# Kernel optimization log

Measured on AMD Instinct MI355X. Metric: run time of the kernel, lower is better.

The kernel has to match this reference:

```python
import jax, jax.numpy as jnp
import numpy as np

B, N, H = 4, 4096, 64
T1 = 3072  # num_types = [0, 3072, 1024]


def _xavier(key, shape):
    fan_in, fan_out = shape[1], shape[0]
    lim = float(np.sqrt(6.0 / (fan_in + fan_out)))
    return jax.random.uniform(key, shape, jnp.float32, -lim, lim)


def setup_inputs() -> dict:
    key = jax.random.key(0)
    ks = jax.random.split(key, 16)
    adjacency = (jax.random.uniform(ks[0], (N, N)) < 0.05).astype(jnp.float32)
    adjacency = jnp.maximum(adjacency, jnp.eye(N, dtype=jnp.float32))  # avoid all-zero rows
    return {
        "hidden_states": jax.random.normal(ks[1], (B, N, H), jnp.float32),
        "input_states": jax.random.normal(ks[2], (B, 1, 1), jnp.float32),
        "adjacency": adjacency,
        "Wq": _xavier(ks[3], (H, H)),
        "Wk": _xavier(ks[4], (H, H)),
        "Wv": _xavier(ks[5], (H, H)),
        "Wu_inter": _xavier(ks[6], (H, H)),
        "bu_inter": jnp.zeros((H,), jnp.float32),
        "Wt_inter": _xavier(ks[7], (H, H)),
        "bt_inter": jnp.zeros((H,), jnp.float32),
        "Wu_out": _xavier(ks[8], (H, H)),
        "bu_out": jnp.zeros((H,), jnp.float32),
        "Wt_out": _xavier(ks[9], (H, H)),
        "bt_out": jnp.zeros((H,), jnp.float32),
        "step_size": jnp.float32(0.01),
    }


def reference(hidden_states, input_states, adjacency, Wq, Wk, Wv,
              Wu_inter, bu_inter, Wt_inter, bt_inter,
              Wu_out, bu_out, Wt_out, bt_out, step_size):
    # AccumulatorFunction: adjacency-masked QK^T, L2-norm rows (NOT softmax), aggregate V
    mask = adjacency.T  # [N, N]
    q = hidden_states @ Wq.T  # [B, N, H]
    k = hidden_states @ Wk.T
    v = hidden_states @ Wv.T
    rel = jnp.einsum('bnd,bmd->bnm', q, k) * mask  # [B, N, N]
    rel = rel / jnp.linalg.norm(rel, axis=2, keepdims=True)
    acc = jnp.einsum('bnm,bmd->bnd', rel, v)  # [B, N, H]

    # update_hidden_states with num_types = [0, T1, N - T1]
    def branch(h, a, Wu, bu, Wt, bt):
        dt = 2.0 * jax.nn.sigmoid(h @ Wt.T + bt) - 1.0
        return h + step_size * dt * (a @ Wu.T + bu)

    upd_inter = branch(hidden_states[:, :T1], acc[:, :T1],
                       Wu_inter, bu_inter, Wt_inter, bt_inter)
    upd_out = branch(hidden_states[:, T1:], acc[:, T1:],
                     Wu_out, bu_out, Wt_out, bt_out)
    return jnp.concatenate([upd_inter, upd_out], axis=1)  # [B, N, H]
```

## Files before the change

kernel.cpp:

```cpp
#include <hip/hip_runtime.h>
#include <hip/hip_bf16.h>
#include <math.h>

#define Bb 4
#define Nn 4096
#define Hh 64
#define T1c 3072
#define MC 4

typedef unsigned short ushort_t;
typedef __bf16 bf16x4 __attribute__((ext_vector_type(4)));
typedef __bf16 bf16x8 __attribute__((ext_vector_type(8)));
typedef float floatx4 __attribute__((ext_vector_type(4)));
typedef float floatx16 __attribute__((ext_vector_type(16)));

__device__ ushort_t g_qw[(size_t)Bb * Nn * Hh];
__device__ ushort_t g_kw[(size_t)Bb * Nn * Hh];
__device__ ushort_t g_vt[(size_t)Bb * Nn * Hh];
__device__ ushort_t g_dt[(size_t)Bb * Nn * Hh];
__device__ unsigned long long g_bm[(size_t)Nn * (Nn / 64)];
__device__ float    g_pac[(size_t)Bb * 64 * MC * 64 * 64];
__device__ float    g_pss[(size_t)Bb * 64 * MC * 64];

__device__ __forceinline__ float bf2f(unsigned short u) {
    union { unsigned int i; float f; } c;
    c.i = ((unsigned int)u) << 16;
    return c.f;
}
__device__ __forceinline__ unsigned short f2bf(float f) {
    union { float f; unsigned int i; } c;
    c.f = f;
    unsigned int x = c.i;
    unsigned int r = (x + 0x7fffu + ((x >> 16) & 1u)) >> 16;
    return (unsigned short)r;
}

__device__ __forceinline__ bf16x8 ld8(const void* p, size_t eidx, bool f32) {
    if (f32) {
        const float* fp = (const float*)p + eidx;
        float4 x0 = *(const float4*)fp;
        float4 x1 = *(const float4*)(fp + 4);
        bf16x8 r;
        r[0] = (__bf16)x0.x; r[1] = (__bf16)x0.y; r[2] = (__bf16)x0.z; r[3] = (__bf16)x0.w;
        r[4] = (__bf16)x1.x; r[5] = (__bf16)x1.y; r[6] = (__bf16)x1.z; r[7] = (__bf16)x1.w;
        return r;
    }
    return *(const bf16x8*)((const ushort_t*)p + eidx);
}
__device__ __forceinline__ float ldS(const void* p, size_t eidx, bool f32) {
    return f32 ? ((const float*)p)[eidx] : bf2f(((const ushort_t*)p)[eidx]);
}
__device__ __forceinline__ void stOut(void* p, size_t eidx, float v, bool f32) {
    if (f32) ((float*)p)[eidx] = v;
    else ((ushort_t*)p)[eidx] = f2bf(v);
}

__device__ __forceinline__ floatx4 mfma16(bf16x8 a, bf16x8 b, floatx4 c) {
    return __builtin_amdgcn_mfma_f32_16x16x32_bf16(a, b, c, 0, 0, 0);
}
__device__ __forceinline__ floatx16 mfma32(bf16x8 a, bf16x8 b, floatx16 c) {
    return __builtin_amdgcn_mfma_f32_32x32x16_bf16(a, b, c, 0, 0, 0);
}
__device__ __forceinline__ bf16x8 cat44(bf16x4 lo, bf16x4 hi) {
    bf16x8 r;
    r[0] = lo[0]; r[1] = lo[1]; r[2] = lo[2]; r[3] = lo[3];
    r[4] = hi[0]; r[5] = hi[1]; r[6] = hi[2]; r[7] = hi[3];
    return r;
}

__device__ __forceinline__ float fast_tanh(float x) {
    float e = __expf(-2.0f * fabsf(x));
    float t = (1.0f - e) / (1.0f + e);
    return copysignf(t, x);
}

__global__ __launch_bounds__(256) void qkvt_kernel(
    const void* __restrict__ hid, const void* __restrict__ adj,
    const void* __restrict__ Wq, const void* __restrict__ Wk,
    const void* __restrict__ Wv,
    const void* __restrict__ Wti, const void* __restrict__ bti,
    const void* __restrict__ Wto, const void* __restrict__ bto)
{
    const bool F32 = (*(const unsigned*)adj) == 0x3F800000u;

    const int bi = blockIdx.x;
    const int b = bi >> 8;
    const int n16 = (bi & 255) << 4;
    const int t = threadIdx.x;
    const int wv = t >> 6, lane = t & 63, l16 = lane & 15, quad = lane >> 4;
    const bool inter = (n16 < T1c);

    const void* W = (wv == 0) ? Wq : (wv == 1) ? Wk : (wv == 2) ? Wv
                    : (inter ? Wti : Wto);
    const void* bt = inter ? bti : bto;

    const size_t hbase = ((size_t)(b * Nn + n16 + l16)) * Hh + quad * 8;
    bf16x8 a0 = ld8(hid, hbase, F32);
    bf16x8 a1 = ld8(hid, hbase + 32, F32);
    floatx4 z = {0.f, 0.f, 0.f, 0.f};

    floatx4 c[4];
#pragma unroll
    for (int ti = 0; ti < 4; ++ti) {
        const size_t wrow = (size_t)(ti * 16 + l16) * 64 + quad * 8;
        bf16x8 w0 = ld8(W, wrow, F32);
        bf16x8 w1 = ld8(W, wrow + 32, F32);
        c[ti] = mfma16(a1, w1, mfma16(a0, w0, z));
    }

    if (wv == 0 || wv == 1) {
        ushort_t* dst = (wv == 0) ? g_qw : g_kw;
#pragma unroll
        for (int ti = 0; ti < 4; ++ti)
#pragma unroll
            for (int r = 0; r < 4; ++r)
                dst[((size_t)(b * Nn + n16 + quad * 4 + r)) * 64 + ti * 16 + l16] = f2bf(c[ti][r]);
    } else if (wv == 2) {
#pragma unroll
        for (int ti = 0; ti < 4; ++ti) {
            uint2 pk;
            pk.x = (unsigned)f2bf(c[ti][0]) | ((unsigned)f2bf(c[ti][1]) << 16);
            pk.y = (unsigned)f2bf(c[ti][2]) | ((unsigned)f2bf(c[ti][3]) << 16);
            *(uint2*)&g_vt[((size_t)(b * 64 + ti * 16 + l16)) * Nn + n16 + quad * 4] = pk;
        }
    } else {
#pragma unroll
        for (int ti = 0; ti < 4; ++ti) {
            const float btv = ldS(bt, ti * 16 + l16, F32);
#pragma unroll
            for (int r = 0; r < 4; ++r)
                g_dt[((size_t)(b * Nn + n16 + quad * 4 + r)) * 64 + ti * 16 + l16] =
                    f2bf(fast_tanh(0.5f * (c[ti][r] + btv)));
        }
    }
}

__global__ __launch_bounds__(256) void bm_kernel(const void* __restrict__ adj)
{
    const bool F32 = (*(const unsigned*)adj) == 0x3F800000u;
    const int bi = blockIdx.x;
    const int mt = bi & 63;
    const int nc = bi >> 6;
    const int n = nc * 256 + threadIdx.x;
    const int m0 = mt * 64;

    unsigned long long bits = 0ull;
#pragma unroll 8
    for (int j = 0; j < 64; ++j) {
        const float v = ldS(adj, (size_t)(m0 + j) * Nn + n, F32);
        bits |= (unsigned long long)(v != 0.f) << j;
    }
    g_bm[(size_t)n * 64 + mt] = bits;
}

__global__ __launch_bounds__(256, 4) void attn_part_kernel()
{
    __shared__ __align__(16) unsigned char smem[64 * 72 * 2 * 2 + 256];
    ushort_t* kT  = (ushort_t*)smem;
    ushort_t* vTl = kT + 64 * 72;

    const unsigned* bm32 = (const unsigned*)g_bm;

    const int bi = blockIdx.x;
    const int b  = bi >> 8;
    const int mc = bi & 3;
    const int nt = (bi >> 2) & 63;
    const int n0 = nt << 6;
    const int t = threadIdx.x;
    const int wv = t >> 6, lane = t & 63;
    const int l32 = lane & 31, h = lane >> 5;
    const int nh = wv >> 1, mh = wv & 1;

    bf16x8 qf[4];
#pragma unroll
    for (int i = 0; i < 4; ++i)
        qf[i] = *(const bf16x8*)&g_qw[((size_t)(b * Nn + n0 + nh * 32 + l32)) * 64 + h * 8 + 16 * i];

    floatx16 acc[2];
#pragma unroll
    for (int dt = 0; dt < 2; ++dt)
#pragma unroll
        for (int r = 0; r < 16; ++r) acc[dt][r] = 0.f;
    float ssql = 0.f;

    int srow[2], scol[2];
#pragma unroll
    for (int i = 0; i < 2; ++i) { const int cc = t + 256 * i; srow[i] = cc >> 3; scol[i] = (cc & 7) * 8; }

    for (int it = 0; it < 16; ++it) {
        const int m0 = mc * 1024 + it * 64;

#pragma unroll
        for (int i = 0; i < 2; ++i) {
            *(bf16x8*)&kT[srow[i] * 72 + scol[i]] =
                *(const bf16x8*)&g_kw[((size_t)(b * Nn + m0 + srow[i])) * 64 + scol[i]];
            *(bf16x8*)&vTl[srow[i] * 72 + scol[i]] =
                *(const bf16x8*)&g_vt[((size_t)(b * 64 + srow[i])) * Nn + m0 + scol[i]];
        }
        __syncthreads();

        floatx16 s;
#pragma unroll
        for (int r = 0; r < 16; ++r) s[r] = 0.f;
#pragma unroll
        for (int i = 0; i < 4; ++i) {
            bf16x8 kf = *(const bf16x8*)&kT[(mh * 32 + l32) * 72 + h * 8 + 16 * i];
            s = mfma32(kf, qf[i], s);
        }

        const unsigned mw = bm32[(size_t)(n0 + nh * 32 + l32) * 128 + mc * 32 + it * 2 + mh];
        bf16x8 af0, af1;
#pragma unroll
        for (int r = 0; r < 16; ++r) {
            const int rp = (r & 3) + 8 * (r >> 2) + 4 * h;
            const float sm = ((mw >> rp) & 1u) ? s[r] : 0.f;
            ssql += sm * sm;
            if (r < 8) af0[r] = (__bf16)sm; else af1[r - 8] = (__bf16)sm;
        }

#pragma unroll
        for (int dt = 0; dt < 2; ++dt) {
            const int vrow = (dt * 32 + l32) * 72 + mh * 32 + 4 * h;
            bf16x4 lo0 = *(const bf16x4*)&vTl[vrow];
            bf16x4 hi0 = *(const bf16x4*)&vTl[vrow + 8];
            acc[dt] = mfma32(af0, cat44(lo0, hi0), acc[dt]);
            bf16x4 lo1 = *(const bf16x4*)&vTl[vrow + 16];
            bf16x4 hi1 = *(const bf16x4*)&vTl[vrow + 16 + 8];
            acc[dt] = mfma32(af1, cat44(lo1, hi1), acc[dt]);
        }
        __syncthreads();
    }

    ssql += __shfl_xor(ssql, 32, 64);

    float* accbuf = (float*)smem;
    float* ssqbuf = (float*)(smem + 16384);
    if (mh == 1) {
#pragma unroll
        for (int dt = 0; dt < 2; ++dt)
#pragma unroll
            for (int r = 0; r < 16; ++r) {
                const int rp = (r & 3) + 8 * (r >> 2) + 4 * h;
                accbuf[((size_t)nh * 32 + rp) * 64 + dt * 32 + l32] = acc[dt][r];
            }
        if (h == 0) ssqbuf[nh * 32 + l32] = ssql;
    }
    __syncthreads();
    if (mh == 0) {
        const size_t pbase = ((size_t)(b * 64 + nt) * MC + mc);
#pragma unroll
        for (int dt = 0; dt < 2; ++dt)
#pragma unroll
            for (int r = 0; r < 16; ++r) {
                const int rp = (r & 3) + 8 * (r >> 2) + 4 * h;
                const float v = acc[dt][r] + accbuf[((size_t)nh * 32 + rp) * 64 + dt * 32 + l32];
                g_pac[(pbase * 64 + nh * 32 + rp) * 64 + dt * 32 + l32] = v;
            }
        ssql += ssqbuf[nh * 32 + l32];
        if (h == 0) g_pss[pbase * 64 + nh * 32 + l32] = ssql;
    }
}

__global__ __launch_bounds__(256) void finish_kernel(
    const void* __restrict__ hid, const void* __restrict__ adj,
    const void* __restrict__ Wui, const void* __restrict__ bui,
    const void* __restrict__ Wuo, const void* __restrict__ buo,
    const void* __restrict__ stepp, void* __restrict__ outp)
{
    const bool F32 = (*(const unsigned*)adj) == 0x3F800000u;

    const int bi = blockIdx.x;
    const int b = bi >> 8;
    const int r16 = bi & 255;
    const int n16 = r16 << 4;
    const int nt = r16 >> 2;
    const int nloc0 = (r16 & 3) << 4;
    const int t = threadIdx.x;
    const int wv = t >> 6, lane = t & 63, l16 = lane & 15, quad = lane >> 4;

    const size_t sbase = ((size_t)(b * 64 + nt) * MC + quad) * 64 + nloc0 + l16;
    float sv = g_pss[sbase];
    sv += __shfl_xor(sv, 16, 64);
    sv += __shfl_xor(sv, 32, 64);
    const float inv = (sv > 0.f) ? __frsqrt_rn(sv) : 0.f;

    float s0[8], s1[8];
#pragma unroll
    for (int j = 0; j < 8; ++j) { s0[j] = 0.f; s1[j] = 0.f; }
#pragma unroll
    for (int mcq = 0; mcq < MC; ++mcq) {
        const size_t abase =
            (((size_t)(b * 64 + nt) * MC + mcq) * 64 + nloc0 + l16) * 64 + quad * 8;
        float4 x0 = *(const float4*)&g_pac[abase];
        float4 x1 = *(const float4*)&g_pac[abase + 4];
        float4 y0 = *(const float4*)&g_pac[abase + 32];
        float4 y1 = *(const float4*)&g_pac[abase + 36];
        s0[0] += x0.x; s0[1] += x0.y; s0[2] += x0.z; s0[3] += x0.w;
        s0[4] += x1.x; s0[5] += x1.y; s0[6] += x1.z; s0[7] += x1.w;
        s1[0] += y0.x; s1[1] += y0.y; s1[2] += y0.z; s1[3] += y0.w;
        s1[4] += y1.x; s1[5] += y1.y; s1[6] += y1.z; s1[7] += y1.w;
    }
    bf16x8 ua0, ua1;
#pragma unroll
    for (int j = 0; j < 8; ++j) {
        ua0[j] = (__bf16)(s0[j] * inv);
        ua1[j] = (__bf16)(s1[j] * inv);
    }

    const bool inter = (n16 < T1c);
    const void* Wu = inter ? Wui : Wuo;
    const void* bu = inter ? bui : buo;
    const float step = ldS(stepp, 0, F32);

    const int ti = wv;
    floatx4 z = {0.f, 0.f, 0.f, 0.f};
    const size_t wrow = (size_t)(ti * 16 + l16) * 64 + quad * 8;
    bf16x8 w0 = ld8(Wu, wrow, F32);
    bf16x8 w1 = ld8(Wu, wrow + 32, F32);
    floatx4 u = mfma16(ua1, w1, mfma16(ua0, w0, z));
    const float buv = ldS(bu, ti * 16 + l16, F32);
#pragma unroll
    for (int r = 0; r < 4; ++r) {
        const size_t idx = ((size_t)(b * Nn + n16 + quad * 4 + r)) * 64 + ti * 16 + l16;
        const float hv = ldS(hid, idx, F32);
        const float dtv = bf2f(g_dt[idx]);
        stOut(outp, idx, hv + step * dtv * (u[r] + buv), F32);
    }
}

extern "C" void kernel_launch(void* const* d_in, const int* in_sizes, int n_in,
                              void* d_out, int out_size, void* d_ws, size_t ws_size,
                              hipStream_t stream)
{
    const void* hid = d_in[0];
    const void* adj = d_in[2];
    const void* Wq  = d_in[3];
    const void* Wk  = d_in[4];
    const void* Wv  = d_in[5];
    const void* Wui = d_in[6];
    const void* bui = d_in[7];
    const void* Wti = d_in[8];
    const void* bti = d_in[9];
    const void* Wuo = d_in[10];
    const void* buo = d_in[11];
    const void* Wto = d_in[12];
    const void* bto = d_in[13];
    const void* stepp = d_in[14];

    qkvt_kernel<<<dim3(Bb * (Nn / 16)), dim3(256), 0, stream>>>(
        hid, adj, Wq, Wk, Wv, Wti, bti, Wto, bto);
    bm_kernel<<<dim3(1024), dim3(256), 0, stream>>>(adj);
    attn_part_kernel<<<dim3(Bb * 64 * MC), dim3(256), 0, stream>>>();
    finish_kernel<<<dim3(Bb * (Nn / 16)), dim3(256), 0, stream>>>(
        hid, adj, Wui, bui, Wuo, buo, stepp, d_out);
}
```

Before: 182.9 us.

## Pre-pack K and V in MFMA fragment layout and drop LDS staging in attention

The QKV projection now writes K and V into a packed layout that matches the MFMA operand fragments. Each wave in the attention kernel then loads its K/V operands straight from global memory, with no LDS staging, no __syncthreads and no cross-wave reduction through shared memory. Each wave owns its own 32 query rows, and the key range is split into 8 chunks instead of 4 to keep 1024 blocks. This removes barriers and LDS traffic. In exchange, every wave re-reads K/V from global memory or L2, and the finish kernel has twice as many partials to sum.

```diff
diff --git a/kernel.cpp b/kernel.cpp
--- a/kernel.cpp
+++ b/kernel.cpp
@@ -6,17 +6,16 @@
 #define Nn 4096
 #define Hh 64
 #define T1c 3072
-#define MC 4
+#define MC 8
 
 typedef unsigned short ushort_t;
-typedef __bf16 bf16x4 __attribute__((ext_vector_type(4)));
 typedef __bf16 bf16x8 __attribute__((ext_vector_type(8)));
 typedef float floatx4 __attribute__((ext_vector_type(4)));
 typedef float floatx16 __attribute__((ext_vector_type(16)));
 
 __device__ ushort_t g_qw[(size_t)Bb * Nn * Hh];
-__device__ ushort_t g_kw[(size_t)Bb * Nn * Hh];
-__device__ ushort_t g_vt[(size_t)Bb * Nn * Hh];
+__device__ ushort_t g_kp[(size_t)Bb * Nn * Hh];
+__device__ ushort_t g_vp[(size_t)Bb * Nn * Hh];
 __device__ ushort_t g_dt[(size_t)Bb * Nn * Hh];
 __device__ unsigned long long g_bm[(size_t)Nn * (Nn / 64)];
 __device__ float    g_pac[(size_t)Bb * 64 * MC * 64 * 64];
@@ -61,12 +60,6 @@
 __device__ __forceinline__ floatx16 mfma32(bf16x8 a, bf16x8 b, floatx16 c) {
     return __builtin_amdgcn_mfma_f32_32x32x16_bf16(a, b, c, 0, 0, 0);
 }
-__device__ __forceinline__ bf16x8 cat44(bf16x4 lo, bf16x4 hi) {
-    bf16x8 r;
-    r[0] = lo[0]; r[1] = lo[1]; r[2] = lo[2]; r[3] = lo[3];
-    r[4] = hi[0]; r[5] = hi[1]; r[6] = hi[2]; r[7] = hi[3];
-    return r;
-}
 
 __device__ __forceinline__ float fast_tanh(float x) {
     float e = __expf(-2.0f * fabsf(x));
@@ -108,20 +101,37 @@
         c[ti] = mfma16(a1, w1, mfma16(a0, w0, z));
     }
 
-    if (wv == 0 || wv == 1) {
-        ushort_t* dst = (wv == 0) ? g_qw : g_kw;
+    if (wv == 0) {
 #pragma unroll
         for (int ti = 0; ti < 4; ++ti)
 #pragma unroll
             for (int r = 0; r < 4; ++r)
-                dst[((size_t)(b * Nn + n16 + quad * 4 + r)) * 64 + ti * 16 + l16] = f2bf(c[ti][r]);
+                g_qw[((size_t)(b * Nn + n16 + quad * 4 + r)) * 64 + ti * 16 + l16] = f2bf(c[ti][r]);
+    } else if (wv == 1) {
+#pragma unroll
+        for (int ti = 0; ti < 4; ++ti) {
+            const int d = ti * 16 + l16;
+#pragma unroll
+            for (int r = 0; r < 4; ++r) {
+                const int m = n16 + quad * 4 + r;
+                const size_t idx =
+                    ((((size_t)(b * 128 + (m >> 5)) * 4 + (d >> 4)) * 2 + ((d >> 3) & 1)) * 32
+                     + (m & 31)) * 8 + (d & 7);
+                g_kp[idx] = f2bf(c[ti][r]);
+            }
+        }
     } else if (wv == 2) {
 #pragma unroll
         for (int ti = 0; ti < 4; ++ti) {
-            uint2 pk;
-            pk.x = (unsigned)f2bf(c[ti][0]) | ((unsigned)f2bf(c[ti][1]) << 16);
-            pk.y = (unsigned)f2bf(c[ti][2]) | ((unsigned)f2bf(c[ti][3]) << 16);
-            *(uint2*)&g_vt[((size_t)(b * 64 + ti * 16 + l16)) * Nn + n16 + quad * 4] = pk;
+            const int d = ti * 16 + l16;
+#pragma unroll
+            for (int r = 0; r < 4; ++r) {
+                const int m = n16 + quad * 4 + r;
+                const size_t idx =
+                    ((((size_t)(b * 256 + (m >> 4)) * 2 + (d >> 5)) * 2 + ((m >> 2) & 1)) * 32
+                     + (d & 31)) * 8 + ((m & 3) | ((m >> 1) & 4));
+                g_vp[idx] = f2bf(c[ti][r]);
+            }
         }
     } else {
 #pragma unroll
@@ -155,26 +165,21 @@
 
 __global__ __launch_bounds__(256, 4) void attn_part_kernel()
 {
-    __shared__ __align__(16) unsigned char smem[64 * 72 * 2 * 2 + 256];
-    ushort_t* kT  = (ushort_t*)smem;
-    ushort_t* vTl = kT + 64 * 72;
-
     const unsigned* bm32 = (const unsigned*)g_bm;
 
     const int bi = blockIdx.x;
     const int b  = bi >> 8;
-    const int mc = bi & 3;
-    const int nt = (bi >> 2) & 63;
-    const int n0 = nt << 6;
-    const int t = threadIdx.x;
-    const int wv = t >> 6, lane = t & 63;
+    const int mc = (bi >> 5) & 7;
+    const int jq = bi & 31;
+    const int wv = threadIdx.x >> 6, lane = threadIdx.x & 63;
     const int l32 = lane & 31, h = lane >> 5;
-    const int nh = wv >> 1, mh = wv & 1;
+    const int j = jq * 4 + wv;
+    const int n0w = j * 32;
 
     bf16x8 qf[4];
 #pragma unroll
     for (int i = 0; i < 4; ++i)
-        qf[i] = *(const bf16x8*)&g_qw[((size_t)(b * Nn + n0 + nh * 32 + l32)) * 64 + h * 8 + 16 * i];
+        qf[i] = *(const bf16x8*)&g_qw[((size_t)(b * Nn + n0w + l32)) * 64 + h * 8 + 16 * i];
 
     floatx16 acc[2];
 #pragma unroll
@@ -183,32 +188,20 @@
         for (int r = 0; r < 16; ++r) acc[dt][r] = 0.f;
     float ssql = 0.f;
 
-    int srow[2], scol[2];
-#pragma unroll
-    for (int i = 0; i < 2; ++i) { const int cc = t + 256 * i; srow[i] = cc >> 3; scol[i] = (cc & 7) * 8; }
-
     for (int it = 0; it < 16; ++it) {
-        const int m0 = mc * 1024 + it * 64;
-
-#pragma unroll
-        for (int i = 0; i < 2; ++i) {
-            *(bf16x8*)&kT[srow[i] * 72 + scol[i]] =
-                *(const bf16x8*)&g_kw[((size_t)(b * Nn + m0 + srow[i])) * 64 + scol[i]];
-            *(bf16x8*)&vTl[srow[i] * 72 + scol[i]] =
-                *(const bf16x8*)&g_vt[((size_t)(b * 64 + srow[i])) * Nn + m0 + scol[i]];
-        }
-        __syncthreads();
+        const int mb32 = mc * 16 + it;
 
         floatx16 s;
 #pragma unroll
         for (int r = 0; r < 16; ++r) s[r] = 0.f;
 #pragma unroll
         for (int i = 0; i < 4; ++i) {
-            bf16x8 kf = *(const bf16x8*)&kT[(mh * 32 + l32) * 72 + h * 8 + 16 * i];
+            bf16x8 kf = *(const bf16x8*)&g_kp[
+                ((((size_t)(b * 128 + mb32) * 4 + i) * 2 + h) * 32 + l32) * 8];
             s = mfma32(kf, qf[i], s);
         }
 
-        const unsigned mw = bm32[(size_t)(n0 + nh * 32 + l32) * 128 + mc * 32 + it * 2 + mh];
+        const unsigned mw = bm32[(size_t)(n0w + l32) * 128 + mb32];
         bf16x8 af0, af1;
 #pragma unroll
         for (int r = 0; r < 16; ++r) {
@@ -219,46 +212,33 @@
         }
 
 #pragma unroll
-        for (int dt = 0; dt < 2; ++dt) {
-            const int vrow = (dt * 32 + l32) * 72 + mh * 32 + 4 * h;
-            bf16x4 lo0 = *(const bf16x4*)&vTl[vrow];
-            bf16x4 hi0 = *(const bf16x4*)&vTl[vrow + 8];
-            acc[dt] = mfma32(af0, cat44(lo0, hi0), acc[dt]);
-            bf16x4 lo1 = *(const bf16x4*)&vTl[vrow + 16];
-            bf16x4 hi1 = *(const bf16x4*)&vTl[vrow + 16 + 8];
-            acc[dt] = mfma32(af1, cat44(lo1, hi1), acc[dt]);
-        }
-        __syncthreads();
+        for (int mb = 0; mb < 2; ++mb) {
+            const size_t vb = (((size_t)(b * 256 + mb32 * 2 + mb) * 2) * 2 + h) * 32 * 8;
+            bf16x8 vf0 = *(const bf16x8*)&g_vp[vb + (size_t)l32 * 8];
+            bf16x8 vf1 = *(const bf16x8*)&g_vp[vb + (2 * 32 * 8) + (size_t)l32 * 8];
+            if (mb == 0) {
+                acc[0] = mfma32(af0, vf0, acc[0]);
+                acc[1] = mfma32(af0, vf1, acc[1]);
+            } else {
+                acc[0] = mfma32(af1, vf0, acc[0]);
+                acc[1] = mfma32(af1, vf1, acc[1]);
+            }
+        }
     }
 
     ssql += __shfl_xor(ssql, 32, 64);
 
-    float* accbuf = (float*)smem;
-    float* ssqbuf = (float*)(smem + 16384);
-    if (mh == 1) {
-#pragma unroll
-        for (int dt = 0; dt < 2; ++dt)
-#pragma unroll
-            for (int r = 0; r < 16; ++r) {
-                const int rp = (r & 3) + 8 * (r >> 2) + 4 * h;
-                accbuf[((size_t)nh * 32 + rp) * 64 + dt * 32 + l32] = acc[dt][r];
-            }
-        if (h == 0) ssqbuf[nh * 32 + l32] = ssql;
-    }
-    __syncthreads();
-    if (mh == 0) {
-        const size_t pbase = ((size_t)(b * 64 + nt) * MC + mc);
-#pragma unroll
-        for (int dt = 0; dt < 2; ++dt)
-#pragma unroll
-            for (int r = 0; r < 16; ++r) {
-                const int rp = (r & 3) + 8 * (r >> 2) + 4 * h;
-                const float v = acc[dt][r] + accbuf[((size_t)nh * 32 + rp) * 64 + dt * 32 + l32];
-                g_pac[(pbase * 64 + nh * 32 + rp) * 64 + dt * 32 + l32] = v;
-            }
-        ssql += ssqbuf[nh * 32 + l32];
-        if (h == 0) g_pss[pbase * 64 + nh * 32 + l32] = ssql;
-    }
+    const int nt = n0w >> 6;
+    const int nl0 = (j & 1) * 32;
+    const size_t pbase = ((size_t)(b * 64 + nt) * MC + mc);
+#pragma unroll
+    for (int dt = 0; dt < 2; ++dt)
+#pragma unroll
+        for (int r = 0; r < 16; ++r) {
+            const int rp = (r & 3) + 8 * (r >> 2) + 4 * h;
+            g_pac[(pbase * 64 + nl0 + rp) * 64 + dt * 32 + l32] = acc[dt][r];
+        }
+    if (h == 0) g_pss[pbase * 64 + nl0 + l32] = ssql;
 }
 
 __global__ __launch_bounds__(256) void finish_kernel(
@@ -278,15 +258,15 @@
     const int t = threadIdx.x;
     const int wv = t >> 6, lane = t & 63, l16 = lane & 15, quad = lane >> 4;
 
-    const size_t sbase = ((size_t)(b * 64 + nt) * MC + quad) * 64 + nloc0 + l16;
-    float sv = g_pss[sbase];
+    float sv = g_pss[((size_t)(b * 64 + nt) * MC + quad) * 64 + nloc0 + l16]
+             + g_pss[((size_t)(b * 64 + nt) * MC + quad + 4) * 64 + nloc0 + l16];
     sv += __shfl_xor(sv, 16, 64);
     sv += __shfl_xor(sv, 32, 64);
     const float inv = (sv > 0.f) ? __frsqrt_rn(sv) : 0.f;
 
     float s0[8], s1[8];
 #pragma unroll
-    for (int j = 0; j < 8; ++j) { s0[j] = 0.f; s1[j] = 0.f; }
+    for (int jj = 0; jj < 8; ++jj) { s0[jj] = 0.f; s1[jj] = 0.f; }
 #pragma unroll
     for (int mcq = 0; mcq < MC; ++mcq) {
         const size_t abase =
@@ -302,9 +282,9 @@
     }
     bf16x8 ua0, ua1;
 #pragma unroll
-    for (int j = 0; j < 8; ++j) {
-        ua0[j] = (__bf16)(s0[j] * inv);
-        ua1[j] = (__bf16)(s1[j] * inv);
+    for (int jj = 0; jj < 8; ++jj) {
+        ua0[jj] = (__bf16)(s0[jj] * inv);
+        ua1[jj] = (__bf16)(s1[jj] * inv);
     }
 
     const bool inter = (n16 < T1c);
@@ -350,7 +330,7 @@
     qkvt_kernel<<<dim3(Bb * (Nn / 16)), dim3(256), 0, stream>>>(
         hid, adj, Wq, Wk, Wv, Wti, bti, Wto, bto);
     bm_kernel<<<dim3(1024), dim3(256), 0, stream>>>(adj);
-    attn_part_kernel<<<dim3(Bb * 64 * MC), dim3(256), 0, stream>>>();
+    attn_part_kernel<<<dim3(1024), dim3(256), 0, stream>>>();
     finish_kernel<<<dim3(Bb * (Nn / 16)), dim3(256), 0, stream>>>(
         hid, adj, Wui, bui, Wuo, buo, stepp, d_out);
 }
```

After: 193.1 us. +5.6%, slower.
